# Kernel optimization log

Hardware: AMD Instinct MI355X
Metric: run time of the kernel (lower is better)

Reference implementation:

```python
import jax, jax.numpy as jnp
import numpy as np
from jax import lax

B, N, F, T = 32, 512, 32, 24
K = 3
GC = 64   # gcn_hidden
TC = 64   # temporal_hidden
STRIDE = 1
LN_EPS = 1e-5


def setup_inputs() -> dict:
    key = jax.random.key(0)
    ks = jax.random.split(key, 20)
    inp = {
        "x": jax.random.normal(ks[0], (B, N, F, T), jnp.float32),
        # Chebyshev basis: K kernels of shape [N, N] (leading batch dim of 1 in torch squeezed)
        "cheb": jax.random.normal(ks[1], (K, N, N), jnp.float32) / np.sqrt(N),
        "w_cheb": jax.random.normal(ks[2], (K, F, GC), jnp.float32),
        # spatial attention params
        "sa_wa": jax.random.normal(ks[3], (T,), jnp.float32),
        "sa_wb": jax.random.normal(ks[4], (F, T), jnp.float32),
        "sa_wc": jax.random.normal(ks[5], (F,), jnp.float32),
        "sa_bias": jax.random.normal(ks[6], (1, N, N), jnp.float32),
        "sa_proj": jax.random.normal(ks[7], (N, N), jnp.float32),
        # temporal attention params
        "ta_w1": jax.random.normal(ks[8], (N,), jnp.float32),
        "ta_w2": jax.random.normal(ks[9], (F, N), jnp.float32),
        "ta_w3": jax.random.normal(ks[10], (F,), jnp.float32),
        "ta_bias": jax.random.normal(ks[11], (1, T, T), jnp.float32),
        "ta_proj": jax.random.normal(ks[12], (T, T), jnp.float32),
        # conv params (torch Conv2d layout OIHW)
        "time_w": jax.random.normal(ks[13], (TC, GC, 1, 3), jnp.float32) / np.sqrt(3 * GC),
        "time_b": jax.random.normal(ks[14], (TC,), jnp.float32) * 0.01,
        "skip_w": jax.random.normal(ks[15], (TC, F, 1, 1), jnp.float32) / np.sqrt(F),
        "skip_b": jax.random.normal(ks[16], (TC,), jnp.float32) * 0.01,
        # layernorm over temporal_hidden
        "ln_g": jnp.ones((TC,), jnp.float32),
        "ln_b": jnp.zeros((TC,), jnp.float32),
    }
    return inp


def _forward(x, cheb, w_cheb, sa_wa, sa_wb, sa_wc, sa_bias, sa_proj,
             ta_w1, ta_w2, ta_w3, ta_bias, ta_proj,
             time_w, time_b, skip_w, skip_b, ln_g, ln_b):
    b, n, f, t = x.shape

    # ---- temporal attention (TemporalAttention.forward) ----
    # lhs = ((x.permute(0,3,2,1) @ w1) @ w2) : [B,T,N]
    lhs_t = jnp.einsum('btf,fn->btn', jnp.einsum('bnft,n->btf', x, ta_w1), ta_w2)
    # rhs = w3 @ x : [B,N,T]
    rhs_t = jnp.einsum('f,bnft->bnt', ta_w3, x)
    prod_t = jnp.einsum('btn,bnu->btu', lhs_t, rhs_t)            # [B,T,T]
    E = jnp.einsum('st,btu->bsu', ta_proj, jax.nn.sigmoid(prod_t + ta_bias))
    temp_w = jax.nn.softmax(E, axis=1)                           # [B,T,T]

    # x_temp = (x.view(B,-1,T) @ temp_w).view(B,N,F,T)
    x_temp = jnp.einsum('bnft,btu->bnfu', x, temp_w)

    # ---- spatial attention (SpatialAttention.forward) on x_temp ----
    lhs_s = jnp.einsum('bnf,ft->bnt', jnp.einsum('bnft,t->bnf', x_temp, sa_wa), sa_wb)  # [B,N,T]
    rhs_s = jnp.einsum('f,bnft->bnt', sa_wc, x_temp)             # [B,N,T] (then transposed)
    scores = jnp.einsum('bnt,bmt->bnm', lhs_s, rhs_s)            # [B,N,N]
    attn = jax.nn.sigmoid(scores + sa_bias)
    S = jnp.einsum('nm,bmp->bnp', sa_proj, attn)
    spat = jax.nn.softmax(S, axis=1)                             # [B,N,N]

    # ---- Chebyshev graph conv (vectorized over T, small loop over K) ----
    # per k: agg += (T_k * spat)^T @ x_slice @ W_k ; fused over all t
    y = jnp.zeros((b, n, w_cheb.shape[-1], t), x.dtype)
    for k in range(cheb.shape[0]):
        A = cheb[k][None, :, :] * spat                           # [B,N,N]
        h = jnp.einsum('bmn,bmft->bnft', A, x)                   # (T_k*attn)^T @ x
        y = y + jnp.einsum('bnft,fo->bnot', h, w_cheb[k])
    gcn = jax.nn.relu(y)                                         # [B,N,GC,T]

    # ---- time conv (1x3, pad (0,1), stride (1,STRIDE)) over [B,C,N,T] ----
    dn = ('NCHW', 'OIHW', 'NCHW')
    tc = lax.conv_general_dilated(gcn.transpose(0, 2, 1, 3), time_w,
                                  window_strides=(1, STRIDE),
                                  padding=((0, 0), (1, 1)),
                                  dimension_numbers=dn)
    tc = tc + time_b[None, :, None, None]

    # ---- skip projection (1x1, stride (1,STRIDE)) ----
    sk = lax.conv_general_dilated(x.transpose(0, 2, 1, 3), skip_w,
                                  window_strides=(1, STRIDE),
                                  padding=((0, 0), (0, 0)),
                                  dimension_numbers=dn)
    sk = sk + skip_b[None, :, None, None]

    out = jax.nn.relu(tc + sk).transpose(0, 3, 2, 1)             # [B,T,N,TC]

    # layernorm over last dim (temporal_hidden)
    mu = out.mean(-1, keepdims=True)
    var = ((out - mu) ** 2).mean(-1, keepdims=True)
    ln = (out - mu) * lax.rsqrt(var + LN_EPS) * ln_g + ln_b

    return ln.transpose(0, 2, 3, 1)                              # [B,N,TC,T]


def reference(x, cheb, w_cheb, sa_wa, sa_wb, sa_wc, sa_bias, sa_proj,
              ta_w1, ta_w2, ta_w3, ta_bias, ta_proj,
              time_w, time_b, skip_w, skip_b, ln_g, ln_b):
    return _forward(x, cheb, w_cheb, sa_wa, sa_wb, sa_wc, sa_bias, sa_proj,
                    ta_w1, ta_w2, ta_w3, ta_bias, ta_proj,
                    time_w, time_b, skip_w, skip_b, ln_g, ln_b)
```

## Files before the change

kernel.cpp:

```cpp
#include <hip/hip_runtime.h>
#include <math.h>

#define Bb_ 32
#define Nn_ 512
#define Ff_ 32
#define Tt_ 24
#define GC_ 64
#define TC_ 64

typedef __attribute__((ext_vector_type(8))) short bf16x8;
typedef __attribute__((ext_vector_type(4))) float f32x4;
typedef __attribute__((ext_vector_type(8))) unsigned short u16x8;
typedef __attribute__((ext_vector_type(4))) unsigned short u16x4;

__device__ __forceinline__ float sigmoidf_(float v) { return 1.0f / (1.0f + __expf(-v)); }

__device__ __forceinline__ unsigned short f2bf(float f) {
    unsigned u = __float_as_uint(f);
    u = (u + 0x7fffu + ((u >> 16) & 1u)) >> 16;
    return (unsigned short)u;
}
__device__ __forceinline__ float bf2f(unsigned short h) {
    return __uint_as_float(((unsigned)h) << 16);
}

__device__ __forceinline__ void async16(const void* g, void* l) {
    __builtin_amdgcn_global_load_lds((const __attribute__((address_space(1))) unsigned int*)g,
                                     (__attribute__((address_space(3))) unsigned int*)l,
                                     16, 0, 0);
}

__global__ void ka_tmp(const float* __restrict__ x, const float* __restrict__ w1,
                       float* __restrict__ tmp) {
    int tid = blockIdx.x * blockDim.x + threadIdx.x;
    int t = tid % Tt_;
    int f = (tid / Tt_) % Ff_;
    int b = tid / (Tt_ * Ff_);
    const float* xp = x + ((size_t)b * Nn_ * Ff_ + f) * Tt_ + t;
    float s = 0.f;
    for (int n = 0; n < Nn_; ++n) s += xp[(size_t)n * Ff_ * Tt_] * w1[n];
    tmp[(b * Tt_ + t) * Ff_ + f] = s;
}

__global__ void kb_rhs(const float* __restrict__ x, const float* __restrict__ w3,
                       float* __restrict__ rhs_t) {
    int tid = blockIdx.x * blockDim.x + threadIdx.x;
    int t = tid % Tt_;
    int n = (tid / Tt_) % Nn_;
    int b = tid / (Tt_ * Nn_);
    const float* xp = x + (((size_t)b * Nn_ + n) * Ff_) * Tt_ + t;
    float s = 0.f;
#pragma unroll
    for (int f = 0; f < Ff_; ++f) s += w3[f] * xp[f * Tt_];
    rhs_t[(b * Nn_ + n) * Tt_ + t] = s;
}

__global__ void kc_lhs(const float* __restrict__ tmp, const float* __restrict__ w2,
                       float* __restrict__ lhs_t) {
    int tid = blockIdx.x * blockDim.x + threadIdx.x;
    int n = tid % Nn_;
    int t = (tid / Nn_) % Tt_;
    int b = tid / (Nn_ * Tt_);
    const float* tp = tmp + (b * Tt_ + t) * Ff_;
    float s = 0.f;
#pragma unroll
    for (int f = 0; f < Ff_; ++f) s += tp[f] * w2[f * Nn_ + n];
    lhs_t[(b * Tt_ + t) * Nn_ + n] = s;
}

__global__ __launch_bounds__(576) void kd_temporal(const float* __restrict__ lhs_t,
                                                   const float* __restrict__ rhs_t,
                                                   const float* __restrict__ ta_bias,
                                                   const float* __restrict__ ta_proj,
                                                   float* __restrict__ temp_w) {
    __shared__ float rl[Nn_ * Tt_];
    __shared__ float sg[Tt_ * Tt_];
    __shared__ float Eb[Tt_ * Tt_];
    int b = blockIdx.x;
    int tid = threadIdx.x;
    for (int i = tid; i < Nn_ * Tt_; i += 576) rl[i] = rhs_t[b * Nn_ * Tt_ + i];
    __syncthreads();
    int u = tid % Tt_;
    int t = tid / Tt_;
    const float* lp = lhs_t + (b * Tt_ + t) * Nn_;
    float s = 0.f;
    for (int n = 0; n < Nn_; ++n) s += lp[n] * rl[n * Tt_ + u];
    sg[t * Tt_ + u] = sigmoidf_(s + ta_bias[t * Tt_ + u]);
    __syncthreads();
    float e = 0.f;
#pragma unroll
    for (int k = 0; k < Tt_; ++k) e += ta_proj[t * Tt_ + k] * sg[k * Tt_ + u];
    Eb[t * Tt_ + u] = e;
    __syncthreads();
    if (tid < Tt_) {
        int uu = tid;
        float m = -1e30f;
        for (int s2 = 0; s2 < Tt_; ++s2) m = fmaxf(m, Eb[s2 * Tt_ + uu]);
        float sum = 0.f;
        for (int s2 = 0; s2 < Tt_; ++s2) sum += __expf(Eb[s2 * Tt_ + uu] - m);
        float inv = 1.0f / sum;
        for (int s2 = 0; s2 < Tt_; ++s2)
            temp_w[b * Tt_ * Tt_ + s2 * Tt_ + uu] = __expf(Eb[s2 * Tt_ + uu] - m) * inv;
    }
}

__global__ __launch_bounds__(256) void ke_spatial(const float* __restrict__ x,
                                                  const float* __restrict__ tw,
                                                  const float* __restrict__ sa_wa,
                                                  const float* __restrict__ sa_wb,
                                                  const float* __restrict__ sa_wc,
                                                  float* __restrict__ lhs_s,
                                                  float* __restrict__ rhs_s) {
    __shared__ float xl[Ff_ * Tt_];
    __shared__ float twl[Tt_ * Tt_];
    __shared__ float xtl[Ff_ * Tt_];
    __shared__ float tmp2[Ff_];
    int n = blockIdx.x, b = blockIdx.y, tid = threadIdx.x;
    const float* xp = x + ((size_t)(b * Nn_ + n)) * Ff_ * Tt_;
    for (int i = tid; i < Ff_ * Tt_; i += 256) xl[i] = xp[i];
    for (int i = tid; i < Tt_ * Tt_; i += 256) twl[i] = tw[b * Tt_ * Tt_ + i];
    __syncthreads();
    for (int i = tid; i < Ff_ * Tt_; i += 256) {
        int f = i / Tt_, u = i % Tt_;
        float s = 0.f;
#pragma unroll
        for (int t = 0; t < Tt_; ++t) s += xl[f * Tt_ + t] * twl[t * Tt_ + u];
        xtl[i] = s;
    }
    __syncthreads();
    if (tid < Ff_) {
        float s = 0.f;
#pragma unroll
        for (int t = 0; t < Tt_; ++t) s += xtl[tid * Tt_ + t] * sa_wa[t];
        tmp2[tid] = s;
    }
    __syncthreads();
    if (tid < Tt_) {
        float a = 0.f, r = 0.f;
#pragma unroll
        for (int f = 0; f < Ff_; ++f) {
            a += tmp2[f] * sa_wb[f * Tt_ + tid];
            r += sa_wc[f] * xtl[f * Tt_ + tid];
        }
        int o = (b * Nn_ + n) * Tt_ + tid;
        lhs_s[o] = a;
        rhs_s[o] = r;
    }
}

__global__ __launch_bounds__(256) void kg_attnT(const float* __restrict__ lhs_s,
                                                const float* __restrict__ rhs_s,
                                                const float* __restrict__ sa_bias,
                                                unsigned short* __restrict__ aTh,
                                                unsigned short* __restrict__ aTl) {
    __shared__ float L[256 * 25];
    __shared__ float R[16 * Tt_];
    __shared__ float Bt[256 * 17];
    int b = blockIdx.y, tid = threadIdx.x;
    int p0 = (blockIdx.x >> 1) * 16;
    int m0 = (blockIdx.x & 1) * 256;
    for (int i = tid; i < 256 * Tt_; i += 256) {
        int m = i / Tt_, t = i - m * Tt_;
        L[m * 25 + t] = lhs_s[b * Nn_ * Tt_ + (m0 + m) * Tt_ + t];
    }
    for (int i = tid; i < 16 * Tt_; i += 256) R[i] = rhs_s[b * Nn_ * Tt_ + p0 * Tt_ + i];
    for (int i = tid; i < 256 * 16; i += 256) {
        int m = i >> 4, j = i & 15;
        Bt[m * 17 + j] = sa_bias[(size_t)(m0 + m) * Nn_ + p0 + j];
    }
    __syncthreads();
    for (int idx = tid; idx < 16 * 256; idx += 256) {
        int r = idx >> 8, mm = idx & 255;
        const float* lp = L + mm * 25;
        const float* rp = R + r * Tt_;
        float s = 0.f;
#pragma unroll
        for (int t = 0; t < Tt_; ++t) s += lp[t] * rp[t];
        float v = sigmoidf_(s + Bt[mm * 17 + r]);
        unsigned short hi = f2bf(v);
        size_t o = ((size_t)b * Nn_ + p0 + r) * Nn_ + m0 + mm;
        aTh[o] = hi;
        aTl[o] = f2bf(v - bf2f(hi));
    }
}

__global__ void kprojsplit(const float* __restrict__ proj,
                           unsigned short* __restrict__ pBh,
                           unsigned short* __restrict__ pBl) {
    int i = blockIdx.x * 256 + threadIdx.x;
    float v = proj[i];
    unsigned short hi = f2bf(v);
    pBh[i] = hi;
    pBl[i] = f2bf(v - bf2f(hi));
}

__global__ __launch_bounds__(256) void kchebT(const float* __restrict__ cheb,
                                              float* __restrict__ chebT) {
    __shared__ float tl[64][65];
    int p0 = blockIdx.x * 64, m0 = blockIdx.y * 64, k = blockIdx.z;
    int tid = threadIdx.x, j = tid & 63, i4 = tid >> 6;
#pragma unroll
    for (int r = 0; r < 16; ++r) {
        int i = i4 + r * 4;
        tl[i][j] = cheb[(size_t)k * Nn_ * Nn_ + (size_t)(m0 + i) * Nn_ + p0 + j];
    }
    __syncthreads();
#pragma unroll
    for (int r = 0; r < 16; ++r) {
        int pp = i4 + r * 4;
        chebT[(size_t)k * Nn_ * Nn_ + (size_t)(p0 + pp) * Nn_ + m0 + j] = tl[j][pp];
    }
}

__global__ __launch_bounds__(256) void ksgemm_mfma(const unsigned short* __restrict__ aTh,
                                                   const unsigned short* __restrict__ aTl,
                                                   const unsigned short* __restrict__ pBh,
                                                   const unsigned short* __restrict__ pBl,
                                                   float* __restrict__ ST) {
    __shared__ unsigned short Ah[512 * 8], Al[512 * 8], Bh[512 * 8], Bl[512 * 8];
    int b = blockIdx.z;
    int p0 = blockIdx.y * 128, n0 = blockIdx.x * 128;
    int tid = threadIdx.x, wid = tid >> 6, lane = tid & 63;
    int l15 = lane & 15, l4 = lane >> 4;
    int wm = (wid & 1) * 64, wn = (wid >> 1) * 64;
    const unsigned short* Abh = aTh + (size_t)b * Nn_ * Nn_;
    const unsigned short* Abl = aTl + (size_t)b * Nn_ * Nn_;

    int cp0 = wid * 128 + lane, cp1 = cp0 + 64;
    int r0 = cp0 >> 2, k0c = (cp0 & 3) ^ ((r0 >> 1) & 3);
    int r1 = cp1 >> 2, k1c = (cp1 & 3) ^ ((r1 >> 1) & 3);
    const unsigned short* gAh0 = Abh + (size_t)(p0 + r0) * Nn_ + k0c * 8;
    const unsigned short* gAh1 = Abh + (size_t)(p0 + r1) * Nn_ + k1c * 8;
    const unsigned short* gAl0 = Abl + (size_t)(p0 + r0) * Nn_ + k0c * 8;
    const unsigned short* gAl1 = Abl + (size_t)(p0 + r1) * Nn_ + k1c * 8;
    const unsigned short* gBh0 = pBh + (size_t)(n0 + r0) * Nn_ + k0c * 8;
    const unsigned short* gBh1 = pBh + (size_t)(n0 + r1) * Nn_ + k1c * 8;
    const unsigned short* gBl0 = pBl + (size_t)(n0 + r0) * Nn_ + k0c * 8;
    const unsigned short* gBl1 = pBl + (size_t)(n0 + r1) * Nn_ + k1c * 8;
    unsigned short* lAh0 = Ah + (size_t)cp0 * 8;
    unsigned short* lAh1 = Ah + (size_t)cp1 * 8;
    unsigned short* lAl0 = Al + (size_t)cp0 * 8;
    unsigned short* lAl1 = Al + (size_t)cp1 * 8;
    unsigned short* lBh0 = Bh + (size_t)cp0 * 8;
    unsigned short* lBh1 = Bh + (size_t)cp1 * 8;
    unsigned short* lBl0 = Bl + (size_t)cp0 * 8;
    unsigned short* lBl1 = Bl + (size_t)cp1 * 8;

    int ca[4], cb[4];
#pragma unroll
    for (int i = 0; i < 4; ++i) {
        int row = wm + i * 16 + l15;
        ca[i] = row * 4 + (l4 ^ ((row >> 1) & 3));
        row = wn + i * 16 + l15;
        cb[i] = row * 4 + (l4 ^ ((row >> 1) & 3));
    }

    f32x4 acc[4][4];
#pragma unroll
    for (int i = 0; i < 4; ++i)
#pragma unroll
        for (int j = 0; j < 4; ++j) acc[i][j] = (f32x4){0.f, 0.f, 0.f, 0.f};

    for (int ks = 0; ks < 16; ++ks) {
        __syncthreads();
        async16(gAh0 + ks * 32, lAh0);
        async16(gAh1 + ks * 32, lAh1);
        async16(gAl0 + ks * 32, lAl0);
        async16(gAl1 + ks * 32, lAl1);
        async16(gBh0 + ks * 32, lBh0);
        async16(gBh1 + ks * 32, lBh1);
        async16(gBl0 + ks * 32, lBl0);
        async16(gBl1 + ks * 32, lBl1);
        __syncthreads();
        bf16x8 ah[4], al[4], bh[4], bl[4];
#pragma unroll
        for (int i = 0; i < 4; ++i) {
            ah[i] = *(const bf16x8*)(Ah + (size_t)ca[i] * 8);
            al[i] = *(const bf16x8*)(Al + (size_t)ca[i] * 8);
        }
#pragma unroll
        for (int j = 0; j < 4; ++j) {
            bh[j] = *(const bf16x8*)(Bh + (size_t)cb[j] * 8);
            bl[j] = *(const bf16x8*)(Bl + (size_t)cb[j] * 8);
        }
#pragma unroll
        for (int i = 0; i < 4; ++i)
#pragma unroll
            for (int j = 0; j < 4; ++j) {
                acc[i][j] = __builtin_amdgcn_mfma_f32_16x16x32_bf16(ah[i], bh[j], acc[i][j], 0, 0, 0);
                acc[i][j] = __builtin_amdgcn_mfma_f32_16x16x32_bf16(ah[i], bl[j], acc[i][j], 0, 0, 0);
                acc[i][j] = __builtin_amdgcn_mfma_f32_16x16x32_bf16(al[i], bh[j], acc[i][j], 0, 0, 0);
            }
    }

    float* Cb = ST + (size_t)b * Nn_ * Nn_;
#pragma unroll
    for (int i = 0; i < 4; ++i)
#pragma unroll
        for (int j = 0; j < 4; ++j) {
            int p = p0 + wm + i * 16 + l4 * 4;
            int n = n0 + wn + j * 16 + l15;
#pragma unroll
            for (int r = 0; r < 4; ++r)
                Cb[(size_t)(p + r) * Nn_ + n] = acc[i][j][r];
        }
}

__global__ __launch_bounds__(256) void kj3(float* __restrict__ ST) {
    int row = blockIdx.x * 4 + (threadIdx.x >> 6);
    int lane = threadIdx.x & 63;
    float* rp = ST + (size_t)row * Nn_ + lane * 8;
    float4 a = *(const float4*)rp;
    float4 c = *(const float4*)(rp + 4);
    float m = fmaxf(fmaxf(fmaxf(a.x, a.y), fmaxf(a.z, a.w)),
                    fmaxf(fmaxf(c.x, c.y), fmaxf(c.z, c.w)));
#pragma unroll
    for (int off = 32; off > 0; off >>= 1) m = fmaxf(m, __shfl_xor(m, off, 64));
    float e0 = __expf(a.x - m), e1 = __expf(a.y - m), e2 = __expf(a.z - m), e3 = __expf(a.w - m);
    float e4 = __expf(c.x - m), e5 = __expf(c.y - m), e6 = __expf(c.z - m), e7 = __expf(c.w - m);
    float s = e0 + e1 + e2 + e3 + e4 + e5 + e6 + e7;
#pragma unroll
    for (int off = 32; off > 0; off >>= 1) s += __shfl_xor(s, off, 64);
    float inv = 1.0f / s;
    *(float4*)rp = make_float4(e0 * inv, e1 * inv, e2 * inv, e3 * inv);
    *(float4*)(rp + 4) = make_float4(e4 * inv, e5 * inv, e6 * inv, e7 * inv);
}

__global__ void kaT3(const float* __restrict__ ST, const float* __restrict__ chebT,
                     unsigned short* __restrict__ AT) {
    size_t i4 = ((size_t)blockIdx.x * 256 + threadIdx.x) * 4;
    int b = (int)(i4 >> 18);
    int pm = (int)(i4 & 262143);
    float4 s = *(const float4*)(ST + (size_t)b * 262144 + pm);
#pragma unroll
    for (int k = 0; k < 3; ++k) {
        float4 cv = *(const float4*)(chebT + (size_t)k * 262144 + pm);
        u16x4 o;
        o[0] = f2bf(cv.x * s.x);
        o[1] = f2bf(cv.y * s.y);
        o[2] = f2bf(cv.z * s.z);
        o[3] = f2bf(cv.w * s.w);
        *(u16x4*)(AT + (size_t)k * 8388608 + (size_t)b * 262144 + pm) = o;
    }
}

__global__ __launch_bounds__(256) void kxT(const float* __restrict__ x,
                                           unsigned short* __restrict__ XT) {
    __shared__ float tl[64][65];
    int q0 = blockIdx.x * 64, m0 = blockIdx.y * 64, b = blockIdx.z;
    int tid = threadIdx.x, j = tid & 63, i4 = tid >> 6;
#pragma unroll
    for (int r = 0; r < 16; ++r) {
        int i = i4 + r * 4;
        tl[i][j] = x[((size_t)(b * Nn_ + m0 + i)) * 768 + q0 + j];
    }
    __syncthreads();
#pragma unroll
    for (int r = 0; r < 16; ++r) {
        int qq = i4 + r * 4;
        XT[((size_t)b * 768 + q0 + qq) * Nn_ + m0 + j] = f2bf(tl[j][qq]);
    }
}

__global__ __launch_bounds__(256) void hgemm_mfma(const unsigned short* __restrict__ AT,
                                                  const unsigned short* __restrict__ XT,
                                                  unsigned short* __restrict__ H) {
    __shared__ unsigned short As[512 * 8];
    __shared__ unsigned short Bs[512 * 8];
    int b = blockIdx.z;
    int p0 = blockIdx.y * 128;
    int q0 = blockIdx.x * 128;
    int tid = threadIdx.x;
    int wid = tid >> 6, lane = tid & 63;
    int l15 = lane & 15, l4 = lane >> 4;
    int wm = (wid & 1) * 64, wn = (wid >> 1) * 64;
    const unsigned short* Ab = AT + (size_t)b * Nn_ * Nn_;
    const unsigned short* Bb = XT + (size_t)b * 768 * Nn_;

    int cp0 = wid * 128 + lane;
    int cp1 = cp0 + 64;
    int rA0 = cp0 >> 2, kA0 = (cp0 & 3) ^ ((rA0 >> 1) & 3);
    int rA1 = cp1 >> 2, kA1 = (cp1 & 3) ^ ((rA1 >> 1) & 3);
    const unsigned short* gA0 = Ab + (size_t)(p0 + rA0) * Nn_ + kA0 * 8;
    const unsigned short* gA1 = Ab + (size_t)(p0 + rA1) * Nn_ + kA1 * 8;
    const unsigned short* gB0 = Bb + (size_t)(q0 + rA0) * Nn_ + kA0 * 8;
    const unsigned short* gB1 = Bb + (size_t)(q0 + rA1) * Nn_ + kA1 * 8;
    unsigned short* lA0 = As + (size_t)(wid * 128) * 8;
    unsigned short* lA1 = As + (size_t)(wid * 128 + 64) * 8;
    unsigned short* lB0 = Bs + (size_t)(wid * 128) * 8;
    unsigned short* lB1 = Bs + (size_t)(wid * 128 + 64) * 8;

    int ca[4], cb[4];
#pragma unroll
    for (int i = 0; i < 4; ++i) {
        int row = wm + i * 16 + l15;
        ca[i] = row * 4 + (l4 ^ ((row >> 1) & 3));
        row = wn + i * 16 + l15;
        cb[i] = row * 4 + (l4 ^ ((row >> 1) & 3));
    }

    f32x4 acc[4][4];
#pragma unroll
    for (int i = 0; i < 4; ++i)
#pragma unroll
        for (int j = 0; j < 4; ++j) acc[i][j] = (f32x4){0.f, 0.f, 0.f, 0.f};

    for (int ks = 0; ks < 16; ++ks) {
        __syncthreads();
        async16(gA0 + ks * 32, lA0);
        async16(gA1 + ks * 32, lA1);
        async16(gB0 + ks * 32, lB0);
        async16(gB1 + ks * 32, lB1);
        __syncthreads();
        bf16x8 af[4], bfv[4];
#pragma unroll
        for (int i = 0; i < 4; ++i) af[i] = *(const bf16x8*)(As + (size_t)ca[i] * 8);
#pragma unroll
        for (int j = 0; j < 4; ++j) bfv[j] = *(const bf16x8*)(Bs + (size_t)cb[j] * 8);
#pragma unroll
        for (int i = 0; i < 4; ++i)
#pragma unroll
            for (int j = 0; j < 4; ++j)
                acc[i][j] = __builtin_amdgcn_mfma_f32_16x16x32_bf16(af[i], bfv[j], acc[i][j], 0, 0, 0);
    }

    unsigned short* Hb = H + (size_t)b * Nn_ * 768;
#pragma unroll
    for (int i = 0; i < 4; ++i)
#pragma unroll
        for (int j = 0; j < 4; ++j) {
            int p = p0 + wm + i * 16 + l4 * 4;
            int q = q0 + wn + j * 16 + l15;
#pragma unroll
            for (int r = 0; r < 4; ++r)
                Hb[(size_t)(p + r) * 768 + q] = f2bf(acc[i][j][r]);
        }
}

__global__ void kprep(const float* __restrict__ wch, const float* __restrict__ skw,
                      const float* __restrict__ tw,
                      unsigned short* __restrict__ WA, unsigned short* __restrict__ WC) {
    int tid = threadIdx.x;
    for (int i = tid; i < 64 * 128; i += 256) {
        int r = i >> 7, kf = i & 127;
        float v = (kf < 96) ? wch[kf * 64 + r] : skw[r * 32 + (kf - 96)];
        WA[i] = f2bf(v);
    }
    for (int i = tid; i < 192 * 64; i += 256) {
        int j = i / 4096, c = (i >> 6) & 63, g = i & 63;
        WC[i] = f2bf(tw[c * 192 + g * 3 + j]);
    }
}

#define HS_ 12582912
#define HLP_ 136
#define GLP_ 72
#define TLP_ 68
__global__ __launch_bounds__(256) void ktail(const unsigned short* __restrict__ H,
                                             const float* __restrict__ x,
                                             const unsigned short* __restrict__ WA,
                                             const unsigned short* __restrict__ WC,
                                             const float* __restrict__ time_b,
                                             const float* __restrict__ skip_b,
                                             const float* __restrict__ ln_g,
                                             const float* __restrict__ ln_b,
                                             float* __restrict__ out) {
    __shared__ __align__(16) char pool_[96 * HLP_ * 2];
    __shared__ __align__(16) unsigned short Gl[104 * GLP_];
    __shared__ float biasS[64], lgS[64], lbS[64];
    __shared__ float muS[96], rsS[96];
    unsigned short* Hl = (unsigned short*)pool_;
    float* Tl = (float*)pool_;

    int b = blockIdx.y;
    int n0 = blockIdx.x * 4;
    size_t bn0 = (size_t)b * Nn_ + n0;
    int tid = threadIdx.x;
    int w = tid >> 6, lane = tid & 63, l15 = lane & 15, l4 = lane >> 4;

    bf16x8 af[4], cf[3][2];
#pragma unroll
    for (int q = 0; q < 4; ++q)
        af[q] = *(const bf16x8*)(WA + (size_t)(16 * w + l15) * 128 + q * 32 + l4 * 8);
#pragma unroll
    for (int j = 0; j < 3; ++j)
#pragma unroll
        for (int kc = 0; kc < 2; ++kc)
            cf[j][kc] = *(const bf16x8*)(WC + (size_t)(j * 64 + 16 * w + l15) * 64 + kc * 32 + l4 * 8);

    for (int c = tid; c < 1152; c += 256) {
        int n = c / 288, rem = c % 288, k = rem / 96, i8 = rem % 96;
        int f = i8 / 3, t0 = (i8 % 3) * 8;
        u16x8 hv = *(const u16x8*)(H + (size_t)k * HS_ + (bn0 + n) * 768 + f * 24 + t0);
#pragma unroll
        for (int s = 0; s < 8; ++s)
            Hl[(n * 24 + t0 + s) * HLP_ + k * 32 + f] = hv[s];
    }
    for (int c = tid; c < 768; c += 256) {
        int n = c / 192, i4 = c % 192, f = i4 / 6, t0 = (i4 % 6) * 4;
        float4 xv = *(const float4*)(x + (bn0 + n) * 768 + f * 24 + t0);
        int base = (n * 24 + t0) * HLP_ + 96 + f;
        Hl[base] = f2bf(xv.x);
        Hl[base + HLP_] = f2bf(xv.y);
        Hl[base + 2 * HLP_] = f2bf(xv.z);
        Hl[base + 3 * HLP_] = f2bf(xv.w);
    }
    for (int i = tid; i < 512; i += 256) {
        int n = i >> 7, r = (i >> 6) & 1, g = i & 63;
        Gl[(n * 26 + r * 25) * GLP_ + g] = 0;
    }
    if (tid < 64) {
        biasS[tid] = time_b[tid] + skip_b[tid];
        lgS[tid] = ln_g[tid];
        lbS[tid] = ln_b[tid];
    }
    __syncthreads();

    f32x4 accs[6];
#pragma unroll
    for (int ct = 0; ct < 6; ++ct) {
        int col = ct * 16 + l15;
        const unsigned short* hr = Hl + col * HLP_ + l4 * 8;
        bf16x8 h0 = *(const bf16x8*)(hr);
        bf16x8 h1 = *(const bf16x8*)(hr + 32);
        bf16x8 h2 = *(const bf16x8*)(hr + 64);
        bf16x8 h3 = *(const bf16x8*)(hr + 96);
        f32x4 g = (f32x4){0.f, 0.f, 0.f, 0.f};
        g = __builtin_amdgcn_mfma_f32_16x16x32_bf16(af[0], h0, g, 0, 0, 0);
        g = __builtin_amdgcn_mfma_f32_16x16x32_bf16(af[1], h1, g, 0, 0, 0);
        g = __builtin_amdgcn_mfma_f32_16x16x32_bf16(af[2], h2, g, 0, 0, 0);
        f32x4 s = (f32x4){0.f, 0.f, 0.f, 0.f};
        s = __builtin_amdgcn_mfma_f32_16x16x32_bf16(af[3], h3, s, 0, 0, 0);
        accs[ct] = s;
        int n = col / 24, t = col - n * 24;
        u16x4 pk;
#pragma unroll
        for (int r = 0; r < 4; ++r) pk[r] = f2bf(g[r] > 0.f ? g[r] : 0.f);
        *(u16x4*)(Gl + (n * 26 + t + 1) * GLP_ + 16 * w + 4 * l4) = pk;
    }
    __syncthreads();

#pragma unroll
    for (int ct = 0; ct < 6; ++ct) {
        int col = ct * 16 + l15;
        int n = col / 24, t = col - n * 24;
        f32x4 acc = accs[ct];
#pragma unroll
        for (int j = 0; j < 3; ++j) {
            const unsigned short* gr = Gl + (n * 26 + t + j) * GLP_ + l4 * 8;
            acc = __builtin_amdgcn_mfma_f32_16x16x32_bf16(cf[j][0], *(const bf16x8*)(gr), acc, 0, 0, 0);
            acc = __builtin_amdgcn_mfma_f32_16x16x32_bf16(cf[j][1], *(const bf16x8*)(gr + 32), acc, 0, 0, 0);
        }
        int cb = 16 * w + 4 * l4;
        f32x4 bv = *(const f32x4*)(biasS + cb);
        f32x4 o;
#pragma unroll
        for (int r = 0; r < 4; ++r) {
            float v = acc[r] + bv[r];
            o[r] = v > 0.f ? v : 0.f;
        }
        *(f32x4*)(Tl + col * TLP_ + cb) = o;
    }
    __syncthreads();

    if (tid < 96) {
        const float* tr = Tl + tid * TLP_;
        float sum = 0.f, sq = 0.f;
#pragma unroll
        for (int i = 0; i < 16; ++i) {
            f32x4 v = *(const f32x4*)(tr + 4 * i);
#pragma unroll
            for (int r = 0; r < 4; ++r) {
                sum += v[r];
                sq += v[r] * v[r];
            }
        }
        float mu = sum * (1.0f / 64.0f);
        float var = sq * (1.0f / 64.0f) - mu * mu;
        muS[tid] = mu;
        rsS[tid] = rsqrtf(var + 1e-5f);
    }
    __syncthreads();

    float* ob = out + bn0 * (TC_ * Tt_);
    for (int idx = tid; idx < 6144; idx += 256) {
        int t = idx % 24;
        int c = (idx / 24) & 63;
        int n = idx / 1536;
        int col = n * 24 + t;
        float v = Tl[col * TLP_ + c];
        ob[idx] = (v - muS[col]) * rsS[col] * lgS[c] + lbS[c];
    }
}

extern "C" void kernel_launch(void* const* d_in, const int* in_sizes, int n_in,
                              void* d_out, int out_size, void* d_ws, size_t ws_size,
                              hipStream_t stream) {
    const float* x       = (const float*)d_in[0];
    const float* cheb    = (const float*)d_in[1];
    const float* w_cheb  = (const float*)d_in[2];
    const float* sa_wa   = (const float*)d_in[3];
    const float* sa_wb   = (const float*)d_in[4];
    const float* sa_wc   = (const float*)d_in[5];
    const float* sa_bias = (const float*)d_in[6];
    const float* sa_proj = (const float*)d_in[7];
    const float* ta_w1   = (const float*)d_in[8];
    const float* ta_w2   = (const float*)d_in[9];
    const float* ta_w3   = (const float*)d_in[10];
    const float* ta_bias = (const float*)d_in[11];
    const float* ta_proj = (const float*)d_in[12];
    const float* time_w  = (const float*)d_in[13];
    const float* time_b  = (const float*)d_in[14];
    const float* skip_w  = (const float*)d_in[15];
    const float* skip_b  = (const float*)d_in[16];
    const float* ln_g    = (const float*)d_in[17];
    const float* ln_b    = (const float*)d_in[18];
    float* out = (float*)d_out;

    float* cur   = (float*)d_ws;
    float* tmp   = cur;            cur += 24576;
    float* lhs_t = cur;            cur += 393216;
    float* rhs_t = cur;            cur += 393216;
    float* tw    = cur;            cur += 18432;
    float* lhs_s = cur;            cur += 393216;
    float* rhs_s = cur;            cur += 393216;
    unsigned short* WAbuf = (unsigned short*)cur;
    unsigned short* WCbuf = WAbuf + 8192;
    cur += 10240;
    unsigned short* pBh = (unsigned short*)cur;
    unsigned short* pBl = pBh + 262144;
    cur += 262144;
    float* chebT = cur;            cur += 786432;
    unsigned short* regionA = (unsigned short*)cur;
    unsigned short* aTh = regionA;
    unsigned short* aTl = regionA + 8388608;
    unsigned short* ATb = regionA;
    cur += 12582912;
    float* STbuf = cur;            cur += 8388608;
    unsigned short* XT = (unsigned short*)cur;
    cur += 6291456;
    unsigned short* hbuf = (unsigned short*)cur;

    kprep<<<1, 256, 0, stream>>>(w_cheb, skip_w, time_w, WAbuf, WCbuf);
    kprojsplit<<<1024, 256, 0, stream>>>(sa_proj, pBh, pBl);
    kchebT<<<dim3(8, 8, 3), 256, 0, stream>>>(cheb, chebT);
    kxT<<<dim3(12, 8, 32), 256, 0, stream>>>(x, XT);
    ka_tmp<<<96, 256, 0, stream>>>(x, ta_w1, tmp);
    kb_rhs<<<1536, 256, 0, stream>>>(x, ta_w3, rhs_t);
    kc_lhs<<<1536, 256, 0, stream>>>(tmp, ta_w2, lhs_t);
    kd_temporal<<<32, 576, 0, stream>>>(lhs_t, rhs_t, ta_bias, ta_proj, tw);
    ke_spatial<<<dim3(512, 32), 256, 0, stream>>>(x, tw, sa_wa, sa_wb, sa_wc, lhs_s, rhs_s);
    kg_attnT<<<dim3(64, 32), 256, 0, stream>>>(lhs_s, rhs_s, sa_bias, aTh, aTl);
    ksgemm_mfma<<<dim3(4, 4, 32), 256, 0, stream>>>(aTh, aTl, pBh, pBl, STbuf);
    kj3<<<4096, 256, 0, stream>>>(STbuf);
    kaT3<<<8192, 256, 0, stream>>>(STbuf, chebT, ATb);
    for (int k = 0; k < 3; ++k) {
        hgemm_mfma<<<dim3(6, 4, 32), 256, 0, stream>>>(ATb + (size_t)k * 8388608, XT,
                                                       hbuf + (size_t)k * HS_);
    }
    ktail<<<dim3(128, 32), 256, 0, stream>>>(hbuf, x, WAbuf, WCbuf,
                                             time_b, skip_b, ln_g, ln_b, out);
}
```

Before: 569.0 us.

## Fuse temporal reductions, softmax with cheb scaling, batch hgemm, swizzle tail LDS

Merges the two x-reduction kernels into one block-tiled kernel that reads x once and accumulates the w1 reduction with atomics, zeroing tmp in kprep. Fuses the row softmax with the Chebyshev multiply and bf16 conversion, so ST is no longer written back and reread. Launches the three per-k hgemm calls as a single grid over 96 z-slices. Replaces the padded LDS layouts in the tail kernel with XOR-swizzled ones and vectorized staging to cut bank conflicts and LDS footprint, at the cost of float atomics that make tmp summation order nondeterministic.

```diff
diff --git a/kernel.cpp b/kernel.cpp
--- a/kernel.cpp
+++ b/kernel.cpp
@@ -7,6 +7,7 @@
 #define Tt_ 24
 #define GC_ 64
 #define TC_ 64
+#define HS_ 12582912
 
 typedef __attribute__((ext_vector_type(8))) short bf16x8;
 typedef __attribute__((ext_vector_type(4))) float f32x4;
@@ -30,29 +31,47 @@
                                      16, 0, 0);
 }
 
-__global__ void ka_tmp(const float* __restrict__ x, const float* __restrict__ w1,
-                       float* __restrict__ tmp) {
-    int tid = blockIdx.x * blockDim.x + threadIdx.x;
-    int t = tid % Tt_;
-    int f = (tid / Tt_) % Ff_;
-    int b = tid / (Tt_ * Ff_);
-    const float* xp = x + ((size_t)b * Nn_ * Ff_ + f) * Tt_ + t;
-    float s = 0.f;
-    for (int n = 0; n < Nn_; ++n) s += xp[(size_t)n * Ff_ * Tt_] * w1[n];
-    tmp[(b * Tt_ + t) * Ff_ + f] = s;
-}
-
-__global__ void kb_rhs(const float* __restrict__ x, const float* __restrict__ w3,
-                       float* __restrict__ rhs_t) {
-    int tid = blockIdx.x * blockDim.x + threadIdx.x;
-    int t = tid % Tt_;
-    int n = (tid / Tt_) % Nn_;
-    int b = tid / (Tt_ * Nn_);
-    const float* xp = x + (((size_t)b * Nn_ + n) * Ff_) * Tt_ + t;
-    float s = 0.f;
-#pragma unroll
-    for (int f = 0; f < Ff_; ++f) s += w3[f] * xp[f * Tt_];
-    rhs_t[(b * Nn_ + n) * Tt_ + t] = s;
+__global__ __launch_bounds__(256) void kab(const float* __restrict__ x,
+                                           const float* __restrict__ w1,
+                                           const float* __restrict__ w3,
+                                           float* __restrict__ tmp,
+                                           float* __restrict__ rhs_t) {
+    __shared__ float xr[768];
+    __shared__ float w3S[32];
+    int b = blockIdx.y, n0 = blockIdx.x * 32, tid = threadIdx.x;
+    if (tid < 32) w3S[tid] = w3[tid];
+    float a0 = 0.f, a1 = 0.f, a2 = 0.f;
+    for (int it = 0; it < 32; ++it) {
+        int n = n0 + it;
+        const float* xp = x + ((size_t)(b * Nn_ + n)) * 768;
+        float v0 = xp[tid], v1 = xp[tid + 256], v2 = xp[tid + 512];
+        float w = w1[n];
+        a0 += w * v0;
+        a1 += w * v1;
+        a2 += w * v2;
+        __syncthreads();
+        xr[tid] = v0;
+        xr[tid + 256] = v1;
+        xr[tid + 512] = v2;
+        __syncthreads();
+        if (tid < 24) {
+            float s = 0.f;
+#pragma unroll
+            for (int f = 0; f < 32; ++f) s += w3S[f] * xr[f * 24 + tid];
+            rhs_t[(b * Nn_ + n) * Tt_ + tid] = s;
+        }
+    }
+    {
+        int i = tid;
+        int f = i / 24, t = i - f * 24;
+        atomicAdd(tmp + b * 768 + t * 32 + f, a0);
+        i = tid + 256;
+        f = i / 24; t = i - f * 24;
+        atomicAdd(tmp + b * 768 + t * 32 + f, a1);
+        i = tid + 512;
+        f = i / 24; t = i - f * 24;
+        atomicAdd(tmp + b * 768 + t * 32 + f, a2);
+    }
 }
 
 __global__ void kc_lhs(const float* __restrict__ tmp, const float* __restrict__ w2,
@@ -306,41 +325,41 @@
         }
 }
 
-__global__ __launch_bounds__(256) void kj3(float* __restrict__ ST) {
+__global__ __launch_bounds__(256) void kjaT(const float* __restrict__ ST,
+                                            const float* __restrict__ chebT,
+                                            unsigned short* __restrict__ AT) {
     int row = blockIdx.x * 4 + (threadIdx.x >> 6);
     int lane = threadIdx.x & 63;
-    float* rp = ST + (size_t)row * Nn_ + lane * 8;
+    const float* rp = ST + (size_t)row * Nn_ + lane * 8;
     float4 a = *(const float4*)rp;
     float4 c = *(const float4*)(rp + 4);
     float m = fmaxf(fmaxf(fmaxf(a.x, a.y), fmaxf(a.z, a.w)),
                     fmaxf(fmaxf(c.x, c.y), fmaxf(c.z, c.w)));
 #pragma unroll
     for (int off = 32; off > 0; off >>= 1) m = fmaxf(m, __shfl_xor(m, off, 64));
-    float e0 = __expf(a.x - m), e1 = __expf(a.y - m), e2 = __expf(a.z - m), e3 = __expf(a.w - m);
-    float e4 = __expf(c.x - m), e5 = __expf(c.y - m), e6 = __expf(c.z - m), e7 = __expf(c.w - m);
-    float s = e0 + e1 + e2 + e3 + e4 + e5 + e6 + e7;
+    float e[8];
+    e[0] = __expf(a.x - m); e[1] = __expf(a.y - m); e[2] = __expf(a.z - m); e[3] = __expf(a.w - m);
+    e[4] = __expf(c.x - m); e[5] = __expf(c.y - m); e[6] = __expf(c.z - m); e[7] = __expf(c.w - m);
+    float s = e[0] + e[1] + e[2] + e[3] + e[4] + e[5] + e[6] + e[7];
 #pragma unroll
     for (int off = 32; off > 0; off >>= 1) s += __shfl_xor(s, off, 64);
     float inv = 1.0f / s;
-    *(float4*)rp = make_float4(e0 * inv, e1 * inv, e2 * inv, e3 * inv);
-    *(float4*)(rp + 4) = make_float4(e4 * inv, e5 * inv, e6 * inv, e7 * inv);
-}
-
-__global__ void kaT3(const float* __restrict__ ST, const float* __restrict__ chebT,
-                     unsigned short* __restrict__ AT) {
-    size_t i4 = ((size_t)blockIdx.x * 256 + threadIdx.x) * 4;
-    int b = (int)(i4 >> 18);
-    int pm = (int)(i4 & 262143);
-    float4 s = *(const float4*)(ST + (size_t)b * 262144 + pm);
+#pragma unroll
+    for (int i = 0; i < 8; ++i) e[i] *= inv;
+    int b = row >> 9, p = row & 511;
 #pragma unroll
     for (int k = 0; k < 3; ++k) {
-        float4 cv = *(const float4*)(chebT + (size_t)k * 262144 + pm);
-        u16x4 o;
-        o[0] = f2bf(cv.x * s.x);
-        o[1] = f2bf(cv.y * s.y);
-        o[2] = f2bf(cv.z * s.z);
-        o[3] = f2bf(cv.w * s.w);
-        *(u16x4*)(AT + (size_t)k * 8388608 + (size_t)b * 262144 + pm) = o;
+        const float* cp = chebT + (size_t)k * 262144 + (size_t)p * Nn_ + lane * 8;
+        float4 c0 = *(const float4*)cp;
+        float4 c1 = *(const float4*)(cp + 4);
+        u16x4 o0, o1;
+        o0[0] = f2bf(c0.x * e[0]); o0[1] = f2bf(c0.y * e[1]);
+        o0[2] = f2bf(c0.z * e[2]); o0[3] = f2bf(c0.w * e[3]);
+        o1[0] = f2bf(c1.x * e[4]); o1[1] = f2bf(c1.y * e[5]);
+        o1[2] = f2bf(c1.z * e[6]); o1[3] = f2bf(c1.w * e[7]);
+        unsigned short* op = AT + (size_t)k * 8388608 + (size_t)b * 262144 + (size_t)p * Nn_ + lane * 8;
+        *(u16x4*)op = o0;
+        *(u16x4*)(op + 4) = o1;
     }
 }
 
@@ -367,14 +386,15 @@
                                                   unsigned short* __restrict__ H) {
     __shared__ unsigned short As[512 * 8];
     __shared__ unsigned short Bs[512 * 8];
-    int b = blockIdx.z;
+    int bz = blockIdx.z;
+    int b = bz & 31, kk2 = bz >> 5;
     int p0 = blockIdx.y * 128;
     int q0 = blockIdx.x * 128;
     int tid = threadIdx.x;
     int wid = tid >> 6, lane = tid & 63;
     int l15 = lane & 15, l4 = lane >> 4;
     int wm = (wid & 1) * 64, wn = (wid >> 1) * 64;
-    const unsigned short* Ab = AT + (size_t)b * Nn_ * Nn_;
+    const unsigned short* Ab = AT + (size_t)kk2 * 8388608 + (size_t)b * Nn_ * Nn_;
     const unsigned short* Bb = XT + (size_t)b * 768 * Nn_;
 
     int cp0 = wid * 128 + lane;
@@ -424,7 +444,7 @@
                 acc[i][j] = __builtin_amdgcn_mfma_f32_16x16x32_bf16(af[i], bfv[j], acc[i][j], 0, 0, 0);
     }
 
-    unsigned short* Hb = H + (size_t)b * Nn_ * 768;
+    unsigned short* Hb = H + (size_t)kk2 * HS_ + (size_t)b * Nn_ * 768;
 #pragma unroll
     for (int i = 0; i < 4; ++i)
 #pragma unroll
@@ -439,7 +459,8 @@
 
 __global__ void kprep(const float* __restrict__ wch, const float* __restrict__ skw,
                       const float* __restrict__ tw,
-                      unsigned short* __restrict__ WA, unsigned short* __restrict__ WC) {
+                      unsigned short* __restrict__ WA, unsigned short* __restrict__ WC,
+                      float* __restrict__ tmp) {
     int tid = threadIdx.x;
     for (int i = tid; i < 64 * 128; i += 256) {
         int r = i >> 7, kf = i & 127;
@@ -450,12 +471,9 @@
         int j = i / 4096, c = (i >> 6) & 63, g = i & 63;
         WC[i] = f2bf(tw[c * 192 + g * 3 + j]);
     }
-}
-
-#define HS_ 12582912
-#define HLP_ 136
-#define GLP_ 72
-#define TLP_ 68
+    for (int i = tid; i < 24576; i += 256) tmp[i] = 0.f;
+}
+
 __global__ __launch_bounds__(256) void ktail(const unsigned short* __restrict__ H,
                                              const float* __restrict__ x,
                                              const unsigned short* __restrict__ WA,
@@ -465,8 +483,8 @@
                                              const float* __restrict__ ln_g,
                                              const float* __restrict__ ln_b,
                                              float* __restrict__ out) {
-    __shared__ __align__(16) char pool_[96 * HLP_ * 2];
-    __shared__ __align__(16) unsigned short Gl[104 * GLP_];
+    __shared__ __align__(16) char pool_[24576];
+    __shared__ __align__(16) unsigned short Gl[104 * 64];
     __shared__ float biasS[64], lgS[64], lbS[64];
     __shared__ float muS[96], rsS[96];
     unsigned short* Hl = (unsigned short*)pool_;
@@ -488,28 +506,49 @@
         for (int kc = 0; kc < 2; ++kc)
             cf[j][kc] = *(const bf16x8*)(WC + (size_t)(j * 64 + 16 * w + l15) * 64 + kc * 32 + l4 * 8);
 
-    for (int c = tid; c < 1152; c += 256) {
-        int n = c / 288, rem = c % 288, k = rem / 96, i8 = rem % 96;
-        int f = i8 / 3, t0 = (i8 % 3) * 8;
-        u16x8 hv = *(const u16x8*)(H + (size_t)k * HS_ + (bn0 + n) * 768 + f * 24 + t0);
-#pragma unroll
-        for (int s = 0; s < 8; ++s)
-            Hl[(n * 24 + t0 + s) * HLP_ + k * 32 + f] = hv[s];
-    }
-    for (int c = tid; c < 768; c += 256) {
-        int n = c / 192, i4 = c % 192, f = i4 / 6, t0 = (i4 % 6) * 4;
-        float4 xv = *(const float4*)(x + (bn0 + n) * 768 + f * 24 + t0);
-        int base = (n * 24 + t0) * HLP_ + 96 + f;
-        Hl[base] = f2bf(xv.x);
-        Hl[base + HLP_] = f2bf(xv.y);
-        Hl[base + 2 * HLP_] = f2bf(xv.z);
-        Hl[base + 3 * HLP_] = f2bf(xv.w);
-    }
-    for (int i = tid; i < 512; i += 256) {
-        int n = i >> 7, r = (i >> 6) & 1, g = i & 63;
-        Gl[(n * 26 + r * 25) * GLP_ + g] = 0;
+#pragma unroll
+    for (int i = 0; i < 3; ++i) {
+        int u = i * 256 + tid;
+        int tg = u % 6;
+        int r1 = u / 6;
+        int n = r1 & 3;
+        int r2 = r1 >> 2;
+        int fg = r2 & 7;
+        int k = r2 >> 3;
+        int t0 = tg * 4, f0 = fg * 4;
+        u16x4 a0, a1, a2, a3;
+        if (k < 3) {
+            const unsigned short* hp = H + (size_t)k * HS_ + (bn0 + n) * 768 + f0 * 24 + t0;
+            a0 = *(const u16x4*)hp;
+            a1 = *(const u16x4*)(hp + 24);
+            a2 = *(const u16x4*)(hp + 48);
+            a3 = *(const u16x4*)(hp + 72);
+        } else {
+            const float* xp = x + (bn0 + n) * 768 + f0 * 24 + t0;
+            float4 v0 = *(const float4*)xp;
+            float4 v1 = *(const float4*)(xp + 24);
+            float4 v2 = *(const float4*)(xp + 48);
+            float4 v3 = *(const float4*)(xp + 72);
+            a0 = (u16x4){f2bf(v0.x), f2bf(v0.y), f2bf(v0.z), f2bf(v0.w)};
+            a1 = (u16x4){f2bf(v1.x), f2bf(v1.y), f2bf(v1.z), f2bf(v1.w)};
+            a2 = (u16x4){f2bf(v2.x), f2bf(v2.y), f2bf(v2.z), f2bf(v2.w)};
+            a3 = (u16x4){f2bf(v3.x), f2bf(v3.y), f2bf(v3.z), f2bf(v3.w)};
+        }
+        int kc4 = k * 4 + (fg >> 1);
+        int half = fg & 1;
+#pragma unroll
+        for (int s = 0; s < 4; ++s) {
+            int col = n * 24 + t0 + s;
+            int pos = col * 16 + (kc4 ^ (col & 7));
+            u16x4 o = (u16x4){a0[s], a1[s], a2[s], a3[s]};
+            *(u16x4*)(Hl + pos * 8 + half * 4) = o;
+        }
     }
     if (tid < 64) {
+        int n = tid >> 4, rr = (tid >> 3) & 1, gc = tid & 7;
+        int row = n * 26 + rr * 25;
+        int posg = row * 8 + (gc ^ (row & 7));
+        *(float4*)(void*)(Gl + posg * 8) = make_float4(0.f, 0.f, 0.f, 0.f);
         biasS[tid] = time_b[tid] + skip_b[tid];
         lgS[tid] = ln_g[tid];
         lbS[tid] = ln_b[tid];
@@ -520,11 +559,11 @@
 #pragma unroll
     for (int ct = 0; ct < 6; ++ct) {
         int col = ct * 16 + l15;
-        const unsigned short* hr = Hl + col * HLP_ + l4 * 8;
-        bf16x8 h0 = *(const bf16x8*)(hr);
-        bf16x8 h1 = *(const bf16x8*)(hr + 32);
-        bf16x8 h2 = *(const bf16x8*)(hr + 64);
-        bf16x8 h3 = *(const bf16x8*)(hr + 96);
+        int cx = col & 7;
+        bf16x8 h0 = *(const bf16x8*)(Hl + (col * 16 + ((0 + l4) ^ cx)) * 8);
+        bf16x8 h1 = *(const bf16x8*)(Hl + (col * 16 + ((4 + l4) ^ cx)) * 8);
+        bf16x8 h2 = *(const bf16x8*)(Hl + (col * 16 + ((8 + l4) ^ cx)) * 8);
+        bf16x8 h3 = *(const bf16x8*)(Hl + (col * 16 + ((12 + l4) ^ cx)) * 8);
         f32x4 g = (f32x4){0.f, 0.f, 0.f, 0.f};
         g = __builtin_amdgcn_mfma_f32_16x16x32_bf16(af[0], h0, g, 0, 0, 0);
         g = __builtin_amdgcn_mfma_f32_16x16x32_bf16(af[1], h1, g, 0, 0, 0);
@@ -533,10 +572,13 @@
         s = __builtin_amdgcn_mfma_f32_16x16x32_bf16(af[3], h3, s, 0, 0, 0);
         accs[ct] = s;
         int n = col / 24, t = col - n * 24;
+        int row = n * 26 + t + 1;
+        int gc = 2 * w + (l4 >> 1);
+        int posg = row * 8 + (gc ^ (row & 7));
         u16x4 pk;
 #pragma unroll
         for (int r = 0; r < 4; ++r) pk[r] = f2bf(g[r] > 0.f ? g[r] : 0.f);
-        *(u16x4*)(Gl + (n * 26 + t + 1) * GLP_ + 16 * w + 4 * l4) = pk;
+        *(u16x4*)(Gl + posg * 8 + (l4 & 1) * 4) = pk;
     }
     __syncthreads();
 
@@ -547,9 +589,12 @@
         f32x4 acc = accs[ct];
 #pragma unroll
         for (int j = 0; j < 3; ++j) {
-            const unsigned short* gr = Gl + (n * 26 + t + j) * GLP_ + l4 * 8;
-            acc = __builtin_amdgcn_mfma_f32_16x16x32_bf16(cf[j][0], *(const bf16x8*)(gr), acc, 0, 0, 0);
-            acc = __builtin_amdgcn_mfma_f32_16x16x32_bf16(cf[j][1], *(const bf16x8*)(gr + 32), acc, 0, 0, 0);
+            int row = n * 26 + t + j;
+            int rx = row & 7;
+            bf16x8 g0 = *(const bf16x8*)(Gl + (row * 8 + (l4 ^ rx)) * 8);
+            bf16x8 g1 = *(const bf16x8*)(Gl + (row * 8 + ((l4 + 4) ^ rx)) * 8);
+            acc = __builtin_amdgcn_mfma_f32_16x16x32_bf16(cf[j][0], g0, acc, 0, 0, 0);
+            acc = __builtin_amdgcn_mfma_f32_16x16x32_bf16(cf[j][1], g1, acc, 0, 0, 0);
         }
         int cb = 16 * w + 4 * l4;
         f32x4 bv = *(const f32x4*)(biasS + cb);
@@ -559,16 +604,18 @@
             float v = acc[r] + bv[r];
             o[r] = v > 0.f ? v : 0.f;
         }
-        *(f32x4*)(Tl + col * TLP_ + cb) = o;
+        int cc = 4 * w + l4;
+        int post = col * 16 + (cc ^ (col & 7));
+        *(f32x4*)(Tl + post * 4) = o;
     }
     __syncthreads();
 
     if (tid < 96) {
-        const float* tr = Tl + tid * TLP_;
         float sum = 0.f, sq = 0.f;
 #pragma unroll
         for (int i = 0; i < 16; ++i) {
-            f32x4 v = *(const f32x4*)(tr + 4 * i);
+            int pos = tid * 16 + (i ^ (tid & 7));
+            f32x4 v = *(const f32x4*)(Tl + pos * 4);
 #pragma unroll
             for (int r = 0; r < 4; ++r) {
                 sum += v[r];
@@ -588,7 +635,8 @@
         int c = (idx / 24) & 63;
         int n = idx / 1536;
         int col = n * 24 + t;
-        float v = Tl[col * TLP_ + c];
+        int pos = col * 16 + ((c >> 2) ^ (col & 7));
+        float v = Tl[pos * 4 + (c & 3)];
         ob[idx] = (v - muS[col]) * rsS[col] * lgS[c] + lbS[c];
     }
 }
@@ -641,23 +689,18 @@
     cur += 6291456;
     unsigned short* hbuf = (unsigned short*)cur;
 
-    kprep<<<1, 256, 0, stream>>>(w_cheb, skip_w, time_w, WAbuf, WCbuf);
+    kprep<<<1, 256, 0, stream>>>(w_cheb, skip_w, time_w, WAbuf, WCbuf, tmp);
     kprojsplit<<<1024, 256, 0, stream>>>(sa_proj, pBh, pBl);
     kchebT<<<dim3(8, 8, 3), 256, 0, stream>>>(cheb, chebT);
     kxT<<<dim3(12, 8, 32), 256, 0, stream>>>(x, XT);
-    ka_tmp<<<96, 256, 0, stream>>>(x, ta_w1, tmp);
-    kb_rhs<<<1536, 256, 0, stream>>>(x, ta_w3, rhs_t);
+    kab<<<dim3(16, 32), 256, 0, stream>>>(x, ta_w1, ta_w3, tmp, rhs_t);
     kc_lhs<<<1536, 256, 0, stream>>>(tmp, ta_w2, lhs_t);
     kd_temporal<<<32, 576, 0, stream>>>(lhs_t, rhs_t, ta_bias, ta_proj, tw);
     ke_spatial<<<dim3(512, 32), 256, 0, stream>>>(x, tw, sa_wa, sa_wb, sa_wc, lhs_s, rhs_s);
     kg_attnT<<<dim3(64, 32), 256, 0, stream>>>(lhs_s, rhs_s, sa_bias, aTh, aTl);
     ksgemm_mfma<<<dim3(4, 4, 32), 256, 0, stream>>>(aTh, aTl, pBh, pBl, STbuf);
-    kj3<<<4096, 256, 0, stream>>>(STbuf);
-    kaT3<<<8192, 256, 0, stream>>>(STbuf, chebT, ATb);
-    for (int k = 0; k < 3; ++k) {
-        hgemm_mfma<<<dim3(6, 4, 32), 256, 0, stream>>>(ATb + (size_t)k * 8388608, XT,
-                                                       hbuf + (size_t)k * HS_);
-    }
+    kjaT<<<4096, 256, 0, stream>>>(STbuf, chebT, ATb);
+    hgemm_mfma<<<dim3(6, 4, 96), 256, 0, stream>>>(ATb, XT, hbuf);
     ktail<<<dim3(128, 32), 256, 0, stream>>>(hbuf, x, WAbuf, WCbuf,
                                              time_b, skip_b, ln_g, ln_b, out);
 }
```

After: 506.6 us. -11.0%, faster.
